# Optimization experiments

Hardware: AMD Instinct MI355X
Metric: run time of the kernel (lower is better)

Reference implementation:

```python
import jax, jax.numpy as jnp
import numpy as np

N, D_IN, D_OUT = 8192, 128, 128

def setup_inputs() -> dict:
    key = jax.random.key(0)
    k1, k2, k3 = jax.random.split(key, 3)
    x = jax.random.normal(k1, (N, D_IN), dtype=jnp.float32)
    adjacency_matrix = jax.random.uniform(k2, (N, N), dtype=jnp.float32)
    weight = jax.random.normal(k3, (D_IN, D_OUT), dtype=jnp.float32) * (1.0 / np.sqrt(D_IN))
    return {"x": x, "adjacency_matrix": adjacency_matrix, "weight": weight}

def reference(x, adjacency_matrix, weight):
    # degree = row sums of A; D^{-1} A  ==  row-normalized adjacency.
    # (torch.inverse of the diagonal degree matrix is just 1/degree.)
    degree = jnp.sum(adjacency_matrix, axis=-1, keepdims=True)  # [N, 1]
    # Fuse: out = D^{-1} (A @ x) @ W  -- avoids materializing normalized A? 
    # Faithful math: (D^{-1} A) x W == D^{-1} (A x) W since D^{-1} is diagonal.
    ax = adjacency_matrix @ x                                   # [N, D_IN]
    out = (ax / degree) @ weight                                # [N, D_OUT]
    return out
```

## Files before the change

### kernel.cpp

```cpp
#include <hip/hip_runtime.h>
#include <hip/hip_bf16.h>

#define NN 8192
#define DD 128

typedef __attribute__((ext_vector_type(4))) float f32x4;
typedef __attribute__((ext_vector_type(16))) float f32x16;
typedef __attribute__((ext_vector_type(8))) short bf16x8;
typedef __attribute__((ext_vector_type(4))) short s16x4;

__device__ __forceinline__ short f2bf(float f) {
  __hip_bfloat16 h = __float2bfloat16(f);
  return __builtin_bit_cast(short, h);
}
__device__ __forceinline__ float bf2f(short s) {
  unsigned u = ((unsigned)(unsigned short)s) << 16;
  return __builtin_bit_cast(float, u);
}

__device__ __forceinline__ void async_copy16(void* lds, const void* g) {
  __builtin_amdgcn_global_load_lds(
      (const __attribute__((address_space(1))) void*)g,
      (__attribute__((address_space(3))) void*)lds, 16, 0, 0);
}

__global__ __launch_bounds__(256) void xw_kernel(
    const float* __restrict__ x, const float* __restrict__ W,
    short* __restrict__ yT)
{
  __shared__ float xs[32][129];
  __shared__ float Ws[128 * 128];
  const int t  = threadIdx.x;
  const int k0 = blockIdx.x * 32;

  #pragma unroll
  for (int i = 0; i < 16; ++i) {
    int idx = (i * 256 + t) * 4;
    *(f32x4*)&Ws[idx] = *(const f32x4*)(W + idx);
  }
  #pragma unroll
  for (int i = 0; i < 4; ++i) {
    int idx = i * 256 + t;
    int row = idx >> 5;
    int c4  = (idx & 31) * 4;
    f32x4 v = *(const f32x4*)(x + (size_t)(k0 + row) * DD + c4);
    xs[row][c4 + 0] = v[0]; xs[row][c4 + 1] = v[1];
    xs[row][c4 + 2] = v[2]; xs[row][c4 + 3] = v[3];
  }
  __syncthreads();

  const int kl = t & 31;
  const int g  = t >> 5;
  float acc[16];
  #pragma unroll
  for (int j = 0; j < 16; ++j) acc[j] = 0.f;

  for (int d = 0; d < 128; ++d) {
    float xv = xs[kl][d];
    const float* wr = &Ws[d * 128 + g * 16];
    f32x4 w0 = *(const f32x4*)(wr);
    f32x4 w1 = *(const f32x4*)(wr + 4);
    f32x4 w2 = *(const f32x4*)(wr + 8);
    f32x4 w3 = *(const f32x4*)(wr + 12);
    #pragma unroll
    for (int j = 0; j < 4; ++j) {
      acc[j]      += xv * w0[j];
      acc[4 + j]  += xv * w1[j];
      acc[8 + j]  += xv * w2[j];
      acc[12 + j] += xv * w3[j];
    }
  }
  #pragma unroll
  for (int j = 0; j < 16; ++j) {
    int n = g * 16 + j;
    yT[(size_t)n * NN + k0 + kl] = f2bf(acc[j]);
  }
}

__global__ __launch_bounds__(512, 4) void gcn_main(
    const float* __restrict__ A, const short* __restrict__ yT,
    short* __restrict__ part, float* __restrict__ degpart)
{
  __shared__ float Abuf[2][256 * 32];
  __shared__ short Ybuf[2][128 * 32];

  const int tid = threadIdx.x;
  const int l   = tid & 63;
  const int w   = tid >> 6;
  const int ks  = blockIdx.x & 7;
  const int mg  = blockIdx.x >> 3;
  const int R0  = mg * 256;
  const int kb  = ks * 1024;
  const int l31 = l & 31;
  const int hi  = l >> 5;
  const int wbase = w * 32;

  const int a_rin  = l >> 3;
  const int a_slot = l & 7;
  const float* gA[4];
  #pragma unroll
  for (int i = 0; i < 4; ++i) {
    const int r = wbase + 8 * i + a_rin;
    gA[i] = A + (size_t)(R0 + r) * NN + kb + ((a_slot ^ (r & 7)) << 2);
  }
  const int y_row = w * 16 + (l >> 2);
  const short* gY = yT + (size_t)y_row * NN + kb + (((l & 3) ^ (y_row & 3)) << 3);

  const int arx = l31 & 7;
  int aoff[2][2];
  #pragma unroll
  for (int j = 0; j < 2; ++j)
    #pragma unroll
    for (int q = 0; q < 2; ++q)
      aoff[j][q] = (wbase + l31) * 32 + (((4 * j + 2 * hi + q) ^ arx) << 2);
  int yoff[4][2];
  #pragma unroll
  for (int f = 0; f < 4; ++f)
    #pragma unroll
    for (int j = 0; j < 2; ++j)
      yoff[f][j] = (f * 32 + l31) * 32 + (((2 * j + hi) ^ (l31 & 3)) << 3);

  f32x16 acc[4];
  #pragma unroll
  for (int f = 0; f < 4; ++f) acc[f] = (f32x16)0.f;
  float deg = 0.f;

#define STAGE(buf, step) do {                                           \
    const int _k = (step) * 32;                                         \
    _Pragma("unroll")                                                   \
    for (int _i = 0; _i < 4; ++_i)                                      \
      async_copy16(&Abuf[buf][(wbase + 8 * _i) * 32], gA[_i] + _k);     \
    async_copy16(&Ybuf[buf][w * 512], gY + _k);                         \
  } while (0)

  STAGE(0, 0);
  STAGE(1, 1);

  for (int s = 0; s < 32; ++s) {
    __builtin_amdgcn_sched_barrier(0);
    if (s < 31) asm volatile("s_waitcnt vmcnt(5)" ::: "memory");
    else        asm volatile("s_waitcnt vmcnt(0)" ::: "memory");
    __builtin_amdgcn_sched_barrier(0);
    __builtin_amdgcn_s_barrier();
    __builtin_amdgcn_sched_barrier(0);

    const float* Ab = &Abuf[s & 1][0];
    const short* Yb = &Ybuf[s & 1][0];

    #pragma unroll
    for (int j = 0; j < 2; ++j) {
      f32x4 a0 = *(const f32x4*)&Ab[aoff[j][0]];
      f32x4 a1 = *(const f32x4*)&Ab[aoff[j][1]];

      deg += (a0[0] + a0[1]) + (a0[2] + a0[3])
           + (a1[0] + a1[1]) + (a1[2] + a1[3]);

      bf16x8 a;
      #pragma unroll
      for (int e = 0; e < 4; ++e) {
        a[e]     = f2bf(a0[e]);
        a[4 + e] = f2bf(a1[e]);
      }

      #pragma unroll
      for (int f = 0; f < 4; ++f) {
        bf16x8 b = *(const bf16x8*)&Yb[yoff[f][j]];
        acc[f] = __builtin_amdgcn_mfma_f32_32x32x16_bf16(a, b, acc[f], 0, 0, 0);
      }
    }

    __builtin_amdgcn_sched_barrier(0);
    __builtin_amdgcn_s_barrier();
    __builtin_amdgcn_sched_barrier(0);
    if (s + 2 < 32) STAGE(s & 1, s + 2);
  }
#undef STAGE

  deg += __shfl_xor(deg, 32);
  if (l < 32)
    degpart[(size_t)ks * NN + R0 + wbase + l] = deg;

  short* pb = part + (size_t)ks * NN * DD + (size_t)(R0 + wbase) * DD;
  #pragma unroll
  for (int f = 0; f < 4; ++f)
    #pragma unroll
    for (int r = 0; r < 16; ++r) {
      const int row = (r & 3) + 8 * (r >> 2) + 4 * hi;
      __builtin_nontemporal_store(f2bf(acc[f][r]),
          pb + (size_t)row * DD + f * 32 + l31);
    }
}

__global__ __launch_bounds__(256) void reduce_kernel(
    const short* __restrict__ part, const float* __restrict__ degpart,
    float* __restrict__ out)
{
  const int idx = blockIdx.x * 256 + threadIdx.x;
  const int m   = idx >> 5;
  const int c4  = (idx & 31) * 4;

  float s0 = 0.f, s1 = 0.f, s2 = 0.f, s3 = 0.f, d = 0.f;
  #pragma unroll
  for (int ks = 0; ks < 8; ++ks) {
    s16x4 v = *(const s16x4*)(part + (size_t)ks * NN * DD + (size_t)m * DD + c4);
    s0 += bf2f(v[0]); s1 += bf2f(v[1]); s2 += bf2f(v[2]); s3 += bf2f(v[3]);
    d += degpart[(size_t)ks * NN + m];
  }
  f32x4 r;
  r[0] = s0 / d; r[1] = s1 / d; r[2] = s2 / d; r[3] = s3 / d;
  *(f32x4*)(out + (size_t)m * DD + c4) = r;
}

extern "C" void kernel_launch(void* const* d_in, const int* in_sizes, int n_in,
                              void* d_out, int out_size, void* d_ws, size_t ws_size,
                              hipStream_t stream) {
  const float* x = (const float*)d_in[0];
  const float* A = (const float*)d_in[1];
  const float* W = (const float*)d_in[2];
  float* out = (float*)d_out;

  char* ws = (char*)d_ws;
  short* yT      = (short*)ws;
  short* part    = (short*)(ws + (2u << 20));
  float* degpart = (float*)(ws + (2u << 20) + (16u << 20));

  xw_kernel<<<256, 256, 0, stream>>>(x, W, yT);
  gcn_main<<<256, 512, 0, stream>>>(A, yT, part, degpart);
  reduce_kernel<<<1024, 256, 0, stream>>>(part, degpart, out);
}
```

Before: 90.94 us.

## Split main GEMM into DMA-to-LDS and register-staged kernels over row halves

Replaces the single 512-thread gcn_main kernel with two 256-thread kernels, each covering 4096 rows in 128-row tiles. The first half keeps direct global-to-LDS async copies. The second half loads A and yT into registers and writes them to LDS with a different software pipeline. This looks like an attempt to compare or mix two load paths, but the two launches run back to back on one stream, so they do not overlap, and each launch covers only half the rows.

```diff
diff --git a/kernel.cpp b/kernel.cpp
--- a/kernel.cpp
+++ b/kernel.cpp
@@ -77,11 +77,12 @@
   }
 }
 
-__global__ __launch_bounds__(512, 4) void gcn_main(
+
+__global__ __launch_bounds__(256) void gcn_dma(
     const float* __restrict__ A, const short* __restrict__ yT,
     short* __restrict__ part, float* __restrict__ degpart)
 {
-  __shared__ float Abuf[2][256 * 32];
+  __shared__ float Abuf[2][128 * 32];
   __shared__ short Ybuf[2][128 * 32];
 
   const int tid = threadIdx.x;
@@ -89,7 +90,7 @@
   const int w   = tid >> 6;
   const int ks  = blockIdx.x & 7;
   const int mg  = blockIdx.x >> 3;
-  const int R0  = mg * 256;
+  const int R0  = mg * 128;
   const int kb  = ks * 1024;
   const int l31 = l & 31;
   const int hi  = l >> 5;
@@ -103,8 +104,12 @@
     const int r = wbase + 8 * i + a_rin;
     gA[i] = A + (size_t)(R0 + r) * NN + kb + ((a_slot ^ (r & 7)) << 2);
   }
-  const int y_row = w * 16 + (l >> 2);
-  const short* gY = yT + (size_t)y_row * NN + kb + (((l & 3) ^ (y_row & 3)) << 3);
+  const short* gY[2];
+  #pragma unroll
+  for (int t = 0; t < 2; ++t) {
+    const int r = wbase + 16 * t + (l >> 2);
+    gY[t] = yT + (size_t)r * NN + kb + (((l & 3) ^ (r & 3)) << 3);
+  }
 
   const int arx = l31 & 7;
   int aoff[2][2];
@@ -130,7 +135,9 @@
     _Pragma("unroll")                                                   \
     for (int _i = 0; _i < 4; ++_i)                                      \
       async_copy16(&Abuf[buf][(wbase + 8 * _i) * 32], gA[_i] + _k);     \
-    async_copy16(&Ybuf[buf][w * 512], gY + _k);                         \
+    _Pragma("unroll")                                                   \
+    for (int _t = 0; _t < 2; ++_t)                                      \
+      async_copy16(&Ybuf[buf][(wbase + 16 * _t) * 32], gY[_t] + _k);    \
   } while (0)
 
   STAGE(0, 0);
@@ -138,7 +145,7 @@
 
   for (int s = 0; s < 32; ++s) {
     __builtin_amdgcn_sched_barrier(0);
-    if (s < 31) asm volatile("s_waitcnt vmcnt(5)" ::: "memory");
+    if (s < 31) asm volatile("s_waitcnt vmcnt(6)" ::: "memory");
     else        asm volatile("s_waitcnt vmcnt(0)" ::: "memory");
     __builtin_amdgcn_sched_barrier(0);
     __builtin_amdgcn_s_barrier();
@@ -151,17 +158,11 @@
     for (int j = 0; j < 2; ++j) {
       f32x4 a0 = *(const f32x4*)&Ab[aoff[j][0]];
       f32x4 a1 = *(const f32x4*)&Ab[aoff[j][1]];
-
       deg += (a0[0] + a0[1]) + (a0[2] + a0[3])
            + (a1[0] + a1[1]) + (a1[2] + a1[3]);
-
       bf16x8 a;
       #pragma unroll
-      for (int e = 0; e < 4; ++e) {
-        a[e]     = f2bf(a0[e]);
-        a[4 + e] = f2bf(a1[e]);
-      }
-
+      for (int e = 0; e < 4; ++e) { a[e] = f2bf(a0[e]); a[4 + e] = f2bf(a1[e]); }
       #pragma unroll
       for (int f = 0; f < 4; ++f) {
         bf16x8 b = *(const bf16x8*)&Yb[yoff[f][j]];
@@ -175,6 +176,138 @@
     if (s + 2 < 32) STAGE(s & 1, s + 2);
   }
 #undef STAGE
+
+  deg += __shfl_xor(deg, 32);
+  if (l < 32)
+    degpart[(size_t)ks * NN + R0 + wbase + l] = deg;
+
+  short* pb = part + (size_t)ks * NN * DD + (size_t)(R0 + wbase) * DD;
+  #pragma unroll
+  for (int f = 0; f < 4; ++f)
+    #pragma unroll
+    for (int r = 0; r < 16; ++r) {
+      const int row = (r & 3) + 8 * (r >> 2) + 4 * hi;
+      __builtin_nontemporal_store(f2bf(acc[f][r]),
+          pb + (size_t)row * DD + f * 32 + l31);
+    }
+}
+
+__global__ __launch_bounds__(256) void gcn_reg(
+    const float* __restrict__ A, const short* __restrict__ yT,
+    short* __restrict__ part, float* __restrict__ degpart)
+{
+  __shared__ float Abuf[2][128 * 32];
+  __shared__ short Ybuf[2][128 * 32];
+
+  const int tid = threadIdx.x;
+  const int l   = tid & 63;
+  const int w   = tid >> 6;
+  const int ks  = blockIdx.x & 7;
+  const int mg  = blockIdx.x >> 3;
+  const int R0  = 4096 + mg * 128;
+  const int kb  = ks * 1024;
+  const int l31 = l & 31;
+  const int hi  = l >> 5;
+  const int wbase = w * 32;
+
+  const int srow = wbase + (l >> 1);
+  const int scol = (l & 1) * 16;
+  const float* gAp = A  + (size_t)(R0 + srow) * NN + kb + scol;
+  const short* gYp = yT + (size_t)srow * NN + kb + scol;
+
+  int awoff[4], ywoff[2];
+  #pragma unroll
+  for (int q = 0; q < 4; ++q) {
+    const int g = (l & 1) * 4 + q;
+    awoff[q] = srow * 32 + ((g ^ (srow & 7)) << 2);
+  }
+  #pragma unroll
+  for (int t = 0; t < 2; ++t) {
+    const int g2 = (l & 1) * 2 + t;
+    ywoff[t] = srow * 32 + ((g2 ^ (srow & 3)) << 3);
+  }
+
+  const int arx = l31 & 7;
+  int aoff[2][2];
+  #pragma unroll
+  for (int j = 0; j < 2; ++j)
+    #pragma unroll
+    for (int q = 0; q < 2; ++q)
+      aoff[j][q] = (wbase + l31) * 32 + (((4 * j + 2 * hi + q) ^ arx) << 2);
+  int yoff[4][2];
+  #pragma unroll
+  for (int f = 0; f < 4; ++f)
+    #pragma unroll
+    for (int j = 0; j < 2; ++j)
+      yoff[f][j] = (f * 32 + l31) * 32 + (((2 * j + hi) ^ (l31 & 3)) << 3);
+
+  f32x16 acc[4];
+  #pragma unroll
+  for (int f = 0; f < 4; ++f) acc[f] = (f32x16)0.f;
+  float deg = 0.f;
+
+  f32x4 av0, av1, av2, av3, yv0, yv1;
+
+#define LOADR(step) do {                                                \
+    const float* _a = gAp + (step) * 32;                                \
+    av0 = *(const f32x4*)(_a);      av1 = *(const f32x4*)(_a + 4);      \
+    av2 = *(const f32x4*)(_a + 8);  av3 = *(const f32x4*)(_a + 12);     \
+    const short* _y = gYp + (step) * 32;                                \
+    yv0 = *(const f32x4*)(_y);      yv1 = *(const f32x4*)(_y + 8);      \
+  } while (0)
+
+#define WRITE(buf) do {                                                 \
+    *(f32x4*)&Abuf[buf][awoff[0]] = av0;                                \
+    *(f32x4*)&Abuf[buf][awoff[1]] = av1;                                \
+    *(f32x4*)&Abuf[buf][awoff[2]] = av2;                                \
+    *(f32x4*)&Abuf[buf][awoff[3]] = av3;                                \
+    *(f32x4*)&Ybuf[buf][ywoff[0]] = yv0;                                \
+    *(f32x4*)&Ybuf[buf][ywoff[1]] = yv1;                                \
+  } while (0)
+
+  LOADR(0);
+  WRITE(0);
+  LOADR(1);
+  asm volatile("s_waitcnt lgkmcnt(0)" ::: "memory");
+  __builtin_amdgcn_sched_barrier(0);
+  __builtin_amdgcn_s_barrier();
+
+  for (int s = 0; s < 32; ++s) {
+    __builtin_amdgcn_sched_barrier(0);
+    const float* Ab = &Abuf[s & 1][0];
+    const short* Yb = &Ybuf[s & 1][0];
+
+    #pragma unroll
+    for (int j = 0; j < 2; ++j) {
+      f32x4 a0 = *(const f32x4*)&Ab[aoff[j][0]];
+      f32x4 a1 = *(const f32x4*)&Ab[aoff[j][1]];
+      deg += (a0[0] + a0[1]) + (a0[2] + a0[3])
+           + (a1[0] + a1[1]) + (a1[2] + a1[3]);
+      bf16x8 a;
+      #pragma unroll
+      for (int e = 0; e < 4; ++e) { a[e] = f2bf(a0[e]); a[4 + e] = f2bf(a1[e]); }
+      #pragma unroll
+      for (int f = 0; f < 4; ++f) {
+        bf16x8 b = *(const bf16x8*)&Yb[yoff[f][j]];
+        acc[f] = __builtin_amdgcn_mfma_f32_32x32x16_bf16(a, b, acc[f], 0, 0, 0);
+      }
+    }
+
+    __builtin_amdgcn_sched_barrier(0);
+    __builtin_amdgcn_s_barrier();
+    __builtin_amdgcn_sched_barrier(0);
+    if (s + 1 < 32) {
+      WRITE((s + 1) & 1);
+      __builtin_amdgcn_sched_barrier(0);
+      if (s + 2 < 32) LOADR(s + 2);
+      __builtin_amdgcn_sched_barrier(0);
+      asm volatile("s_waitcnt lgkmcnt(0)" ::: "memory");
+      __builtin_amdgcn_sched_barrier(0);
+    }
+    __builtin_amdgcn_s_barrier();
+  }
+#undef LOADR
+#undef WRITE
 
   deg += __shfl_xor(deg, 32);
   if (l < 32)
@@ -225,6 +358,7 @@
   float* degpart = (float*)(ws + (2u << 20) + (16u << 20));
 
   xw_kernel<<<256, 256, 0, stream>>>(x, W, yT);
-  gcn_main<<<256, 512, 0, stream>>>(A, yT, part, degpart);
+  gcn_dma<<<256, 256, 0, stream>>>(A, yT, part, degpart);
+  gcn_reg<<<256, 256, 0, stream>>>(A, yT, part, degpart);
   reduce_kernel<<<1024, 256, 0, stream>>>(part, degpart, out);
 }
```

New measurement: 98.56 us. 1.08x slower.
